# Kernel tuning notes

Hardware: AMD Instinct MI355X
Metric: run time of the kernel (lower is better)

Reference implementation:

```python
import jax, jax.numpy as jnp
import numpy as np

N = 8192      # nodes
E = 262144    # edges (avg degree 32)
D_IN = 128    # feat dim (out_channels)
D_H = 256     # hidden_channels * 2
D_OUT = 64    # in_channels (final embedding dim)


def _sage_pool(feat, src, dst, n, Wp, bp, Ws, Wn, b, ew):
    # DGL SAGEConv('pool'): h_pool = relu(fc_pool(feat)); msg = h_pool[src] * ew;
    # h_neigh = max over in-edges (0 for isolated nodes);
    # out = fc_self(feat) + fc_neigh(h_neigh) + bias
    h = jax.nn.relu(feat @ Wp + bp)                          # [N, d_in]
    msg = h[src] * ew[:, None]                               # [E, d_in]
    agg = jax.ops.segment_max(msg, dst, num_segments=n)      # [N, d_in], -inf if no in-edges
    agg = jnp.where(jnp.isfinite(agg), agg, 0.0)
    return feat @ Ws + agg @ Wn + b


def setup_inputs() -> dict:
    key = jax.random.key(0)
    ks = jax.random.split(key, 20)
    feat = jax.random.normal(ks[0], (N, D_IN), dtype=jnp.float32)
    src = jax.random.randint(ks[1], (E,), 0, N)
    dst = jax.random.randint(ks[2], (E,), 0, N)
    edge_weight = jax.random.uniform(ks[3], (E,), dtype=jnp.float32)

    def lin(k, din, dout):
        return jax.random.normal(k, (din, dout), dtype=jnp.float32) / np.float32(np.sqrt(din))

    params = {}
    dims = [(D_IN, D_H), (D_H, D_H), (D_H, D_OUT)]
    i = 4
    for l, (di, do) in enumerate(dims, 1):
        params[f"Wp{l}"] = lin(ks[i], di, di); i += 1
        params[f"bp{l}"] = jnp.zeros((di,), jnp.float32)
        params[f"Ws{l}"] = lin(ks[i], di, do); i += 1
        params[f"Wn{l}"] = lin(ks[i], di, do); i += 1
        params[f"b{l}"] = jnp.zeros((do,), jnp.float32)

    return dict(feat=feat, src=src, dst=dst, edge_weight=edge_weight, n_nodes=N, **params)


def reference(feat, src, dst, edge_weight, n_nodes,
              Wp1, bp1, Ws1, Wn1, b1,
              Wp2, bp2, Ws2, Wn2, b2,
              Wp3, bp3, Ws3, Wn3, b3):
    hd = jax.nn.relu(_sage_pool(feat, src, dst, n_nodes, Wp1, bp1, Ws1, Wn1, b1, edge_weight))
    hd = jax.nn.relu(_sage_pool(hd,   src, dst, n_nodes, Wp2, bp2, Ws2, Wn2, b2, edge_weight))
    hd = jax.nn.relu(_sage_pool(hd,   src, dst, n_nodes, Wp3, bp3, Ws3, Wn3, b3, edge_weight))
    adj_rec = hd @ hd.T                                      # [N, N]
    return hd, adj_rec
```

## Files before the change

kernel.cpp:

```cpp
#include <hip/hip_runtime.h>
#include <hip/hip_bf16.h>

#define NN 8192
#define NE 262144

typedef __attribute__((ext_vector_type(8))) __bf16 bf16x8;
typedef __attribute__((ext_vector_type(4))) float f32x4;

__device__ __forceinline__ ushort f2b(float v) {
    __hip_bfloat16 b = __float2bfloat16(v);
    return *reinterpret_cast<ushort*>(&b);
}
__device__ __forceinline__ uint pack2(float lo, float hi) {
    return (uint)f2b(lo) | ((uint)f2b(hi) << 16);
}

struct PrepArgs {
    const float* feat; ushort* featb; int* ptr;
    const float* w[9]; ushort* wt[9];
};

__global__ __launch_bounds__(256) void prep_k(PrepArgs a) {
    const int bid = blockIdx.x, tid = threadIdx.x;
    if (bid < 32) {
        a.ptr[bid * 256 + tid] = 0;
        return;
    }
    if (bid < 32 + 1024) {
        int i = ((bid - 32) * 256 + tid) * 4;
        float4 f = *(const float4*)&a.feat[i];
        uint2 o; o.x = pack2(f.x, f.y); o.y = pack2(f.z, f.w);
        *(uint2*)&a.featb[i] = o;
        return;
    }
    int id = (bid - 1056) * 256 + tid;
    if (id >= 376832) return;
    const int cum[10] = {0, 16384, 49152, 81920, 147456, 212992, 278528, 344064, 360448, 376832};
    const int KK[9] = {128, 128, 128, 256, 256, 256, 256, 256, 256};
    const int LN[9] = {7, 8, 8, 8, 8, 8, 8, 6, 6};
    int m = 0;
#pragma unroll
    for (int t = 1; t < 9; ++t) m += (id >= cum[t]);
    int local = id - cum[m];
    int K = KK[m], ln = LN[m];
    int k = local >> ln, n = local & ((1 << ln) - 1);
    a.wt[m][n * K + k] = f2b(a.w[m][local]);
}

__global__ void count_k(const int* __restrict__ dst, int* __restrict__ cnt) {
    int e = blockIdx.x * blockDim.x + threadIdx.x;
    if (e < NE) atomicAdd(&cnt[dst[e]], 1);
}

__global__ __launch_bounds__(1024) void scan8192_k(int* __restrict__ ptr, int* __restrict__ row_ptr) {
    __shared__ int buf[1024];
    int tid = threadIdx.x;
    int4 va = *(const int4*)&ptr[tid * 8];
    int4 vb = *(const int4*)&ptr[tid * 8 + 4];
    int v[8] = {va.x, va.y, va.z, va.w, vb.x, vb.y, vb.z, vb.w};
    int sum = 0;
#pragma unroll
    for (int i = 0; i < 8; ++i) sum += v[i];
    buf[tid] = sum;
    __syncthreads();
    int acc = sum;
    for (int off = 1; off < 1024; off <<= 1) {
        int t = (tid >= off) ? buf[tid - off] : 0;
        __syncthreads();
        acc += t;
        buf[tid] = acc;
        __syncthreads();
    }
    int run = acc - sum;
    int o[8];
#pragma unroll
    for (int i = 0; i < 8; ++i) { o[i] = run; run += v[i]; }
    *(int4*)&row_ptr[tid * 8] = make_int4(o[0], o[1], o[2], o[3]);
    *(int4*)&row_ptr[tid * 8 + 4] = make_int4(o[4], o[5], o[6], o[7]);
    *(int4*)&ptr[tid * 8] = make_int4(o[0], o[1], o[2], o[3]);
    *(int4*)&ptr[tid * 8 + 4] = make_int4(o[4], o[5], o[6], o[7]);
    if (tid == 1023) row_ptr[NN] = run;
}

__global__ void scatter_k(const int* __restrict__ src, const int* __restrict__ dst,
                          const float* __restrict__ ew, int* __restrict__ ptr,
                          int* __restrict__ csr_src, float* __restrict__ csr_w) {
    int e = blockIdx.x * blockDim.x + threadIdx.x;
    if (e < NE) {
        int p = atomicAdd(&ptr[dst[e]], 1);
        csr_src[p] = src[e];
        csr_w[p] = ew[e];
    }
}

#define TBM 128
#define TBN 64
#define TBK 32
#define AW  40

template <bool DUAL, bool RELU, int OUTMODE>
__global__ __launch_bounds__(256) void gemm_bf16_k(
    const ushort* __restrict__ A1, const ushort* __restrict__ BT1, int K1,
    const ushort* __restrict__ A2, const ushort* __restrict__ BT2, int K2,
    const float* __restrict__ bias, float* __restrict__ Cf, ushort* __restrict__ Cb,
    int M, int N) {
    __shared__ __align__(16) ushort As[TBM * AW];
    __shared__ __align__(16) ushort Bs[TBN * AW];

    int tid = threadIdx.x;
    int lane = tid & 63, wave = tid >> 6;
    int wm = (wave >> 1) * 64, wn = (wave & 1) * 32;
    int r16 = lane & 15, kb = lane >> 4;
    int m0 = blockIdx.y * TBM, n0 = blockIdx.x * TBN;

    f32x4 acc[4][2];
#pragma unroll
    for (int i = 0; i < 4; ++i)
#pragma unroll
        for (int j = 0; j < 2; ++j) acc[i][j] = (f32x4)(0.f);

#pragma unroll 1
    for (int pass = 0; pass < (DUAL ? 2 : 1); ++pass) {
        const ushort* A = pass ? A2 : A1;
        const ushort* BT = pass ? BT2 : BT1;
        int K = pass ? K2 : K1;
        for (int k0 = 0; k0 < K; k0 += TBK) {
#pragma unroll
            for (int rep = 0; rep < 2; ++rep) {
                int id = rep * 256 + tid;
                int row = id >> 2, c = id & 3;
                *(bf16x8*)&As[row * AW + c * 8] =
                    *(const bf16x8*)&A[(size_t)(m0 + row) * K + k0 + c * 8];
            }
            {
                int row = tid >> 2, c = tid & 3;
                *(bf16x8*)&Bs[row * AW + c * 8] =
                    *(const bf16x8*)&BT[(size_t)(n0 + row) * K + k0 + c * 8];
            }
            __syncthreads();
            bf16x8 a[4], b[2];
#pragma unroll
            for (int i = 0; i < 4; ++i)
                a[i] = *(const bf16x8*)&As[(wm + 16 * i + r16) * AW + kb * 8];
#pragma unroll
            for (int j = 0; j < 2; ++j)
                b[j] = *(const bf16x8*)&Bs[(wn + 16 * j + r16) * AW + kb * 8];
#pragma unroll
            for (int i = 0; i < 4; ++i)
#pragma unroll
                for (int j = 0; j < 2; ++j)
                    acc[i][j] = __builtin_amdgcn_mfma_f32_16x16x32_bf16(a[i], b[j], acc[i][j], 0, 0, 0);
            __syncthreads();
        }
    }

#pragma unroll
    for (int i = 0; i < 4; ++i) {
#pragma unroll
        for (int j = 0; j < 2; ++j) {
            int col = n0 + wn + 16 * j + r16;
            float bv = (bias != nullptr) ? bias[col] : 0.f;
#pragma unroll
            for (int r = 0; r < 4; ++r) {
                int row = m0 + wm + 16 * i + kb * 4 + r;
                float v = acc[i][j][r] + bv;
                if (RELU) v = fmaxf(v, 0.f);
                if (OUTMODE != 0) Cf[(size_t)row * N + col] = v;
                if (OUTMODE != 1) Cb[(size_t)row * N + col] = f2b(v);
            }
        }
    }
}

template <int D, int WPN>
__global__ __launch_bounds__(256) void seg_max_k2(
    const ushort* __restrict__ h, const int* __restrict__ row_ptr,
    const int* __restrict__ csr_src, const float* __restrict__ csr_w,
    ushort* __restrict__ agg) {
    int wave = threadIdx.x >> 6, lane = threadIdx.x & 63;
    int node = blockIdx.x * (4 / WPN) + wave / WPN;
    int half = wave % WPN;
    int f0 = half * 128 + lane * 2;
    int e0 = row_ptr[node], e1 = row_ptr[node + 1];
    float mlo = 0.f, mhi = 0.f;

    auto upd = [&](int s, float w) {
        uint u = *(const uint*)&h[(size_t)s * D + f0];
        float lo = __uint_as_float(u << 16);
        float hi = __uint_as_float(u & 0xffff0000u);
        mlo = fmaxf(mlo, lo * w);
        mhi = fmaxf(mhi, hi * w);
    };

    int e = e0;
    for (; e + 4 <= e1; e += 4) {
        int s0 = csr_src[e], s1 = csr_src[e + 1], s2 = csr_src[e + 2], s3 = csr_src[e + 3];
        float w0 = csr_w[e], w1 = csr_w[e + 1], w2 = csr_w[e + 2], w3 = csr_w[e + 3];
        upd(s0, w0); upd(s1, w1); upd(s2, w2); upd(s3, w3);
    }
    for (; e < e1; ++e) upd(csr_src[e], csr_w[e]);

    *(uint*)&agg[(size_t)node * D + f0] = pack2(mlo, mhi);
}

__global__ __launch_bounds__(256) void aat_k(const ushort* __restrict__ H,
                                             float* __restrict__ C) {
    __shared__ __align__(16) ushort As[128 * 72];
    __shared__ __align__(16) ushort Bs[128 * 72];
    int tid = threadIdx.x, lane = tid & 63, wave = tid >> 6;
    int wm = (wave >> 1) * 64, wn = (wave & 1) * 64;
    int r16 = lane & 15, kb = lane >> 4;
    int m0 = blockIdx.y * 128, n0 = blockIdx.x * 128;

#pragma unroll
    for (int rep = 0; rep < 4; ++rep) {
        int id = rep * 256 + tid;
        int row = id >> 3, c = id & 7;
        *(bf16x8*)&As[row * 72 + c * 8] = *(const bf16x8*)&H[(size_t)(m0 + row) * 64 + c * 8];
        *(bf16x8*)&Bs[row * 72 + c * 8] = *(const bf16x8*)&H[(size_t)(n0 + row) * 64 + c * 8];
    }
    __syncthreads();

    f32x4 acc[4][4];
#pragma unroll
    for (int i = 0; i < 4; ++i)
#pragma unroll
        for (int j = 0; j < 4; ++j) acc[i][j] = (f32x4)(0.f);

#pragma unroll
    for (int kc = 0; kc < 2; ++kc) {
        bf16x8 a[4], b[4];
#pragma unroll
        for (int i = 0; i < 4; ++i)
            a[i] = *(const bf16x8*)&As[(wm + 16 * i + r16) * 72 + kc * 32 + kb * 8];
#pragma unroll
        for (int j = 0; j < 4; ++j)
            b[j] = *(const bf16x8*)&Bs[(wn + 16 * j + r16) * 72 + kc * 32 + kb * 8];
#pragma unroll
        for (int i = 0; i < 4; ++i)
#pragma unroll
            for (int j = 0; j < 4; ++j)
                acc[i][j] = __builtin_amdgcn_mfma_f32_16x16x32_bf16(a[i], b[j], acc[i][j], 0, 0, 0);
    }

#pragma unroll
    for (int i = 0; i < 4; ++i) {
#pragma unroll
        for (int j = 0; j < 4; ++j) {
            int col = n0 + wn + 16 * j + r16;
#pragma unroll
            for (int r = 0; r < 4; ++r) {
                size_t row = m0 + wm + 16 * i + kb * 4 + r;
                C[row * NN + col] = acc[i][j][r];
            }
        }
    }
}

extern "C" void kernel_launch(void* const* d_in, const int* in_sizes, int n_in,
                              void* d_out, int out_size, void* d_ws, size_t ws_size,
                              hipStream_t stream) {
    const float* feat = (const float*)d_in[0];
    const int* src = (const int*)d_in[1];
    const int* dst = (const int*)d_in[2];
    const float* ew = (const float*)d_in[3];
    const float* Wp1 = (const float*)d_in[5];
    const float* bp1 = (const float*)d_in[6];
    const float* Ws1 = (const float*)d_in[7];
    const float* Wn1 = (const float*)d_in[8];
    const float* b1  = (const float*)d_in[9];
    const float* Wp2 = (const float*)d_in[10];
    const float* bp2 = (const float*)d_in[11];
    const float* Ws2 = (const float*)d_in[12];
    const float* Wn2 = (const float*)d_in[13];
    const float* b2  = (const float*)d_in[14];
    const float* Wp3 = (const float*)d_in[15];
    const float* bp3 = (const float*)d_in[16];
    const float* Ws3 = (const float*)d_in[17];
    const float* Wn3 = (const float*)d_in[18];
    const float* b3  = (const float*)d_in[19];

    float* out = (float*)d_out;
    float* adj = out + (size_t)NN * 64;

    char* ws = (char*)d_ws;
    int* row_ptr = (int*)(ws + 0x0);
    int* ptr     = (int*)(ws + 0x10000);
    int* csr_src = (int*)(ws + 0x20000);
    float* csr_w = (float*)(ws + 0x120000);
    ushort* featb = (ushort*)(ws + 0x220000);
    ushort* Wp1T = (ushort*)(ws + 0x420000);
    ushort* Ws1T = (ushort*)(ws + 0x428000);
    ushort* Wn1T = (ushort*)(ws + 0x438000);
    ushort* Wp2T = (ushort*)(ws + 0x448000);
    ushort* Ws2T = (ushort*)(ws + 0x468000);
    ushort* Wn2T = (ushort*)(ws + 0x488000);
    ushort* Wp3T = (ushort*)(ws + 0x4A8000);
    ushort* Ws3T = (ushort*)(ws + 0x4C8000);
    ushort* Wn3T = (ushort*)(ws + 0x4D0000);
    ushort* P = (ushort*)(ws + 0x500000);
    ushort* G = (ushort*)(ws + 0x900000);
    ushort* X = (ushort*)(ws + 0xD00000);
    ushort* Y = (ushort*)(ws + 0x1100000);
    ushort* hdb = (ushort*)(ws + 0x1500000);

    PrepArgs pa;
    pa.feat = feat; pa.featb = featb; pa.ptr = ptr;
    const float* wsrc[9] = {Wp1, Ws1, Wn1, Wp2, Ws2, Wn2, Wp3, Ws3, Wn3};
    ushort* wdst[9] = {Wp1T, Ws1T, Wn1T, Wp2T, Ws2T, Wn2T, Wp3T, Ws3T, Wn3T};
    for (int i = 0; i < 9; ++i) { pa.w[i] = wsrc[i]; pa.wt[i] = wdst[i]; }
    prep_k<<<32 + 1024 + 1472, 256, 0, stream>>>(pa);

    count_k<<<NE / 256, 256, 0, stream>>>(dst, ptr);
    scan8192_k<<<1, 1024, 0, stream>>>(ptr, row_ptr);
    scatter_k<<<NE / 256, 256, 0, stream>>>(src, dst, ew, ptr, csr_src, csr_w);

    gemm_bf16_k<false, true, 0><<<dim3(128 / TBN, NN / TBM), 256, 0, stream>>>(
        featb, Wp1T, 128, nullptr, nullptr, 0, bp1, nullptr, P, NN, 128);
    seg_max_k2<128, 1><<<NN / 4, 256, 0, stream>>>(P, row_ptr, csr_src, csr_w, G);
    gemm_bf16_k<true, true, 0><<<dim3(256 / TBN, NN / TBM), 256, 0, stream>>>(
        featb, Ws1T, 128, G, Wn1T, 128, b1, nullptr, X, NN, 256);

    gemm_bf16_k<false, true, 0><<<dim3(256 / TBN, NN / TBM), 256, 0, stream>>>(
        X, Wp2T, 256, nullptr, nullptr, 0, bp2, nullptr, P, NN, 256);
    seg_max_k2<256, 2><<<NN / 2, 256, 0, stream>>>(P, row_ptr, csr_src, csr_w, G);
    gemm_bf16_k<true, true, 0><<<dim3(256 / TBN, NN / TBM), 256, 0, stream>>>(
        X, Ws2T, 256, G, Wn2T, 256, b2, nullptr, Y, NN, 256);

    gemm_bf16_k<false, true, 0><<<dim3(256 / TBN, NN / TBM), 256, 0, stream>>>(
        Y, Wp3T, 256, nullptr, nullptr, 0, bp3, nullptr, P, NN, 256);
    seg_max_k2<256, 2><<<NN / 2, 256, 0, stream>>>(P, row_ptr, csr_src, csr_w, G);
    gemm_bf16_k<true, true, 2><<<dim3(64 / TBN, NN / TBM), 256, 0, stream>>>(
        Y, Ws3T, 256, G, Wn3T, 256, b3, out, hdb, NN, 64);

    aat_k<<<dim3(NN / 128, NN / 128), 256, 0, stream>>>(hdb, adj);
}
```

Measured before the change: 189.9 us.

## Interleave CSR src/weight, widen seg-max per lane, retile GEMMs

The CSR source indices and edge weights are packed into one uint2 array, so each edge costs a single 8-byte load instead of two separate loads. The segment-max kernel now uses one wave per node, with each lane covering 2 or 4 features, and prefetches 8 edges at a time to raise memory-level parallelism. The GEMM kernel is templated on block tile size and relaunched with 64x64 or 64x128 tiles, changing block counts and the work per block. The risks are lower occupancy from more registers per lane in seg-max and different wave counts in the GEMMs.

```diff
diff --git a/kernel.cpp b/kernel.cpp
--- a/kernel.cpp
+++ b/kernel.cpp
@@ -84,40 +84,38 @@
 
 __global__ void scatter_k(const int* __restrict__ src, const int* __restrict__ dst,
                           const float* __restrict__ ew, int* __restrict__ ptr,
-                          int* __restrict__ csr_src, float* __restrict__ csr_w) {
+                          uint2* __restrict__ csr_sw) {
     int e = blockIdx.x * blockDim.x + threadIdx.x;
     if (e < NE) {
         int p = atomicAdd(&ptr[dst[e]], 1);
-        csr_src[p] = src[e];
-        csr_w[p] = ew[e];
-    }
-}
-
-#define TBM 128
-#define TBN 64
+        csr_sw[p] = make_uint2((uint)src[e], __float_as_uint(ew[e]));
+    }
+}
+
 #define TBK 32
 #define AW  40
 
-template <bool DUAL, bool RELU, int OUTMODE>
+template <int BM, int BN, bool DUAL, bool RELU, int OUTMODE>
 __global__ __launch_bounds__(256) void gemm_bf16_k(
     const ushort* __restrict__ A1, const ushort* __restrict__ BT1, int K1,
     const ushort* __restrict__ A2, const ushort* __restrict__ BT2, int K2,
     const float* __restrict__ bias, float* __restrict__ Cf, ushort* __restrict__ Cb,
     int M, int N) {
-    __shared__ __align__(16) ushort As[TBM * AW];
-    __shared__ __align__(16) ushort Bs[TBN * AW];
+    constexpr int MI = BM / 32, NJ = BN / 32;
+    __shared__ __align__(16) ushort As[BM * AW];
+    __shared__ __align__(16) ushort Bs[BN * AW];
 
     int tid = threadIdx.x;
     int lane = tid & 63, wave = tid >> 6;
-    int wm = (wave >> 1) * 64, wn = (wave & 1) * 32;
+    int wm = (wave >> 1) * (BM / 2), wn = (wave & 1) * (BN / 2);
     int r16 = lane & 15, kb = lane >> 4;
-    int m0 = blockIdx.y * TBM, n0 = blockIdx.x * TBN;
-
-    f32x4 acc[4][2];
-#pragma unroll
-    for (int i = 0; i < 4; ++i)
-#pragma unroll
-        for (int j = 0; j < 2; ++j) acc[i][j] = (f32x4)(0.f);
+    int m0 = blockIdx.y * BM, n0 = blockIdx.x * BN;
+
+    f32x4 acc[MI][NJ];
+#pragma unroll
+    for (int i = 0; i < MI; ++i)
+#pragma unroll
+        for (int j = 0; j < NJ; ++j) acc[i][j] = (f32x4)(0.f);
 
 #pragma unroll 1
     for (int pass = 0; pass < (DUAL ? 2 : 1); ++pass) {
@@ -126,38 +124,40 @@
         int K = pass ? K2 : K1;
         for (int k0 = 0; k0 < K; k0 += TBK) {
 #pragma unroll
-            for (int rep = 0; rep < 2; ++rep) {
+            for (int rep = 0; rep < BM / 64; ++rep) {
                 int id = rep * 256 + tid;
                 int row = id >> 2, c = id & 3;
                 *(bf16x8*)&As[row * AW + c * 8] =
                     *(const bf16x8*)&A[(size_t)(m0 + row) * K + k0 + c * 8];
             }
-            {
-                int row = tid >> 2, c = tid & 3;
+#pragma unroll
+            for (int rep = 0; rep < BN / 64; ++rep) {
+                int id = rep * 256 + tid;
+                int row = id >> 2, c = id & 3;
                 *(bf16x8*)&Bs[row * AW + c * 8] =
                     *(const bf16x8*)&BT[(size_t)(n0 + row) * K + k0 + c * 8];
             }
             __syncthreads();
-            bf16x8 a[4], b[2];
-#pragma unroll
-            for (int i = 0; i < 4; ++i)
+            bf16x8 a[MI], b[NJ];
+#pragma unroll
+            for (int i = 0; i < MI; ++i)
                 a[i] = *(const bf16x8*)&As[(wm + 16 * i + r16) * AW + kb * 8];
 #pragma unroll
-            for (int j = 0; j < 2; ++j)
+            for (int j = 0; j < NJ; ++j)
                 b[j] = *(const bf16x8*)&Bs[(wn + 16 * j + r16) * AW + kb * 8];
 #pragma unroll
-            for (int i = 0; i < 4; ++i)
-#pragma unroll
-                for (int j = 0; j < 2; ++j)
+            for (int i = 0; i < MI; ++i)
+#pragma unroll
+                for (int j = 0; j < NJ; ++j)
                     acc[i][j] = __builtin_amdgcn_mfma_f32_16x16x32_bf16(a[i], b[j], acc[i][j], 0, 0, 0);
             __syncthreads();
         }
     }
 
 #pragma unroll
-    for (int i = 0; i < 4; ++i) {
-#pragma unroll
-        for (int j = 0; j < 2; ++j) {
+    for (int i = 0; i < MI; ++i) {
+#pragma unroll
+        for (int j = 0; j < NJ; ++j) {
             int col = n0 + wn + 16 * j + r16;
             float bv = (bias != nullptr) ? bias[col] : 0.f;
 #pragma unroll
@@ -172,35 +172,46 @@
     }
 }
 
-template <int D, int WPN>
-__global__ __launch_bounds__(256) void seg_max_k2(
+template <int D, int FPL>
+__global__ __launch_bounds__(256) void seg_max_k3(
     const ushort* __restrict__ h, const int* __restrict__ row_ptr,
-    const int* __restrict__ csr_src, const float* __restrict__ csr_w,
-    ushort* __restrict__ agg) {
+    const uint2* __restrict__ csr_sw, ushort* __restrict__ agg) {
     int wave = threadIdx.x >> 6, lane = threadIdx.x & 63;
-    int node = blockIdx.x * (4 / WPN) + wave / WPN;
-    int half = wave % WPN;
-    int f0 = half * 128 + lane * 2;
+    int node = blockIdx.x * 4 + wave;
+    int f0 = lane * FPL;
     int e0 = row_ptr[node], e1 = row_ptr[node + 1];
-    float mlo = 0.f, mhi = 0.f;
-
-    auto upd = [&](int s, float w) {
-        uint u = *(const uint*)&h[(size_t)s * D + f0];
-        float lo = __uint_as_float(u << 16);
-        float hi = __uint_as_float(u & 0xffff0000u);
-        mlo = fmaxf(mlo, lo * w);
-        mhi = fmaxf(mhi, hi * w);
+    float mx[FPL];
+#pragma unroll
+    for (int i = 0; i < FPL; ++i) mx[i] = 0.f;
+
+    auto upd = [&](uint s, float w) {
+        const uint* hp = (const uint*)&h[(size_t)s * D + f0];
+#pragma unroll
+        for (int c = 0; c < FPL / 2; ++c) {
+            uint u = hp[c];
+            float lo = __uint_as_float(u << 16);
+            float hi = __uint_as_float(u & 0xffff0000u);
+            mx[2 * c] = fmaxf(mx[2 * c], lo * w);
+            mx[2 * c + 1] = fmaxf(mx[2 * c + 1], hi * w);
+        }
     };
 
     int e = e0;
-    for (; e + 4 <= e1; e += 4) {
-        int s0 = csr_src[e], s1 = csr_src[e + 1], s2 = csr_src[e + 2], s3 = csr_src[e + 3];
-        float w0 = csr_w[e], w1 = csr_w[e + 1], w2 = csr_w[e + 2], w3 = csr_w[e + 3];
-        upd(s0, w0); upd(s1, w1); upd(s2, w2); upd(s3, w3);
-    }
-    for (; e < e1; ++e) upd(csr_src[e], csr_w[e]);
-
-    *(uint*)&agg[(size_t)node * D + f0] = pack2(mlo, mhi);
+    for (; e + 8 <= e1; e += 8) {
+        uint2 d[8];
+#pragma unroll
+        for (int t = 0; t < 8; ++t) d[t] = csr_sw[e + t];
+#pragma unroll
+        for (int t = 0; t < 8; ++t) upd(d[t].x, __uint_as_float(d[t].y));
+    }
+    for (; e < e1; ++e) {
+        uint2 d = csr_sw[e];
+        upd(d.x, __uint_as_float(d.y));
+    }
+
+    uint* ap = (uint*)&agg[(size_t)node * D + f0];
+#pragma unroll
+    for (int c = 0; c < FPL / 2; ++c) ap[c] = pack2(mx[2 * c], mx[2 * c + 1]);
 }
 
 __global__ __launch_bounds__(256) void aat_k(const ushort* __restrict__ H,
@@ -286,8 +297,7 @@
     char* ws = (char*)d_ws;
     int* row_ptr = (int*)(ws + 0x0);
     int* ptr     = (int*)(ws + 0x10000);
-    int* csr_src = (int*)(ws + 0x20000);
-    float* csr_w = (float*)(ws + 0x120000);
+    uint2* csr_sw = (uint2*)(ws + 0x20000);
     ushort* featb = (ushort*)(ws + 0x220000);
     ushort* Wp1T = (ushort*)(ws + 0x420000);
     ushort* Ws1T = (ushort*)(ws + 0x428000);
@@ -313,24 +323,24 @@
 
     count_k<<<NE / 256, 256, 0, stream>>>(dst, ptr);
     scan8192_k<<<1, 1024, 0, stream>>>(ptr, row_ptr);
-    scatter_k<<<NE / 256, 256, 0, stream>>>(src, dst, ew, ptr, csr_src, csr_w);
-
-    gemm_bf16_k<false, true, 0><<<dim3(128 / TBN, NN / TBM), 256, 0, stream>>>(
+    scatter_k<<<NE / 256, 256, 0, stream>>>(src, dst, ew, ptr, csr_sw);
+
+    gemm_bf16_k<64, 64, false, true, 0><<<dim3(2, 128), 256, 0, stream>>>(
         featb, Wp1T, 128, nullptr, nullptr, 0, bp1, nullptr, P, NN, 128);
-    seg_max_k2<128, 1><<<NN / 4, 256, 0, stream>>>(P, row_ptr, csr_src, csr_w, G);
-    gemm_bf16_k<true, true, 0><<<dim3(256 / TBN, NN / TBM), 256, 0, stream>>>(
+    seg_max_k3<128, 2><<<NN / 4, 256, 0, stream>>>(P, row_ptr, csr_sw, G);
+    gemm_bf16_k<64, 128, true, true, 0><<<dim3(2, 128), 256, 0, stream>>>(
         featb, Ws1T, 128, G, Wn1T, 128, b1, nullptr, X, NN, 256);
 
-    gemm_bf16_k<false, true, 0><<<dim3(256 / TBN, NN / TBM), 256, 0, stream>>>(
+    gemm_bf16_k<64, 128, false, true, 0><<<dim3(2, 128), 256, 0, stream>>>(
         X, Wp2T, 256, nullptr, nullptr, 0, bp2, nullptr, P, NN, 256);
-    seg_max_k2<256, 2><<<NN / 2, 256, 0, stream>>>(P, row_ptr, csr_src, csr_w, G);
-    gemm_bf16_k<true, true, 0><<<dim3(256 / TBN, NN / TBM), 256, 0, stream>>>(
+    seg_max_k3<256, 4><<<NN / 4, 256, 0, stream>>>(P, row_ptr, csr_sw, G);
+    gemm_bf16_k<64, 128, true, true, 0><<<dim3(2, 128), 256, 0, stream>>>(
         X, Ws2T, 256, G, Wn2T, 256, b2, nullptr, Y, NN, 256);
 
-    gemm_bf16_k<false, true, 0><<<dim3(256 / TBN, NN / TBM), 256, 0, stream>>>(
+    gemm_bf16_k<64, 128, false, true, 0><<<dim3(2, 128), 256, 0, stream>>>(
         Y, Wp3T, 256, nullptr, nullptr, 0, bp3, nullptr, P, NN, 256);
-    seg_max_k2<256, 2><<<NN / 2, 256, 0, stream>>>(P, row_ptr, csr_src, csr_w, G);
-    gemm_bf16_k<true, true, 2><<<dim3(64 / TBN, NN / TBM), 256, 0, stream>>>(
+    seg_max_k3<256, 4><<<NN / 4, 256, 0, stream>>>(P, row_ptr, csr_sw, G);
+    gemm_bf16_k<64, 64, true, true, 2><<<dim3(1, 128), 256, 0, stream>>>(
         Y, Ws3T, 256, G, Wn3T, 256, b3, out, hdb, NN, 64);
 
     aat_k<<<dim3(NN / 128, NN / 128), 256, 0, stream>>>(hdb, adj);
```

New measurement: 181.4 us. -4.5%, faster.
